# Kernel tuning notes

Measured on AMD Instinct MI355X. Metric: run time of the kernel, lower is better.

The kernel has to match this reference:

```python
import jax, jax.numpy as jnp
import numpy as np


def setup_inputs() -> dict:
    key = jax.random.key(0)
    ks = jax.random.split(key, 7)
    B, T, C, H = 8, 2048, 2048, 128
    x = jax.random.normal(ks[0], (B, T, C), dtype=jnp.float32)
    Wq = jax.random.normal(ks[1], (C, H), dtype=jnp.float32) * (C ** -0.5)
    bq = jax.random.normal(ks[2], (H,), dtype=jnp.float32) * 0.02
    Wk = jax.random.normal(ks[3], (C, H), dtype=jnp.float32) * (C ** -0.5)
    bk = jax.random.normal(ks[4], (H,), dtype=jnp.float32) * 0.02
    Wv = jax.random.normal(ks[5], (C, H), dtype=jnp.float32) * (C ** -0.5)
    bv = jax.random.normal(ks[6], (H,), dtype=jnp.float32) * 0.02
    return {"x": x, "Wq": Wq, "bq": bq, "Wk": Wk, "bk": bk, "Wv": Wv, "bv": bv}


def reference(x, Wq, bq, Wk, bk, Wv, bv):
    # Single-head causal self-attention (dropout in eval mode = identity).
    B, T, C = x.shape
    H = Wq.shape[1]
    Q = jnp.einsum("btc,ch->bth", x, Wq) + bq  # [B,T,H]
    K = jnp.einsum("btc,ch->bth", x, Wk) + bk
    V = jnp.einsum("btc,ch->bth", x, Wv) + bv
    scale = H ** -0.5
    wei = jnp.einsum("bth,bsh->bts", Q, K) * scale  # [B,T,T]
    causal = jnp.tril(jnp.ones((T, T), dtype=bool))
    wei = jnp.where(causal, wei, -jnp.inf)
    wei = jax.nn.softmax(wei, axis=-1)
    out = jnp.einsum("bts,bsh->bth", wei, V)  # [B,T,H]
    return out
```

## Files before the change

kernel.cpp:

```cpp
#include <hip/hip_runtime.h>

typedef float f32x4 __attribute__((ext_vector_type(4)));
typedef short short8 __attribute__((ext_vector_type(8)));
typedef unsigned short ushort8 __attribute__((ext_vector_type(8)));

#define WS_Q  786432
#define WS_K  2883584
#define WS_VT 4980736
#define NITER 64

__device__ __forceinline__ unsigned short f2bf(float x) {
    unsigned u = __float_as_uint(x);
    u += 0x7FFFu + ((u >> 16) & 1u);
    return (unsigned short)(u >> 16);
}

__device__ __forceinline__ int swz128(int row, int cbyte) {
    return row * 128 + (cbyte ^ ((row & 7) << 4));
}

__global__ __launch_bounds__(256) void wt_kernel(const float* __restrict__ Wq,
        const float* __restrict__ Wk, const float* __restrict__ Wv,
        unsigned short* __restrict__ ws) {
    __shared__ __align__(16) unsigned short tile[64][136];
    int mat = blockIdx.x >> 5, ct = blockIdx.x & 31;
    const float* W = (mat == 0) ? Wq : ((mat == 1) ? Wk : Wv);
    int cbase = ct * 64;
    int tid = threadIdx.x;
#pragma unroll
    for (int p = 0; p < 8; p++) {
        int fidx = p * 256 + tid;
        int row = fidx >> 5;
        int c4 = (fidx & 31) << 2;
        float4 v = *(const float4*)&W[(size_t)(cbase + row) * 128 + c4];
        tile[row][c4 + 0] = f2bf(v.x);
        tile[row][c4 + 1] = f2bf(v.y);
        tile[row][c4 + 2] = f2bf(v.z);
        tile[row][c4 + 3] = f2bf(v.w);
    }
    __syncthreads();
    int h = tid >> 1, seg = tid & 1;
    unsigned short* dst = ws + mat * 262144 + (ct * 2 + seg) * 4096 + h * 32;
#pragma unroll
    for (int q4 = 0; q4 < 4; q4++) {
        ushort8 pk;
#pragma unroll
        for (int e = 0; e < 8; e++) pk[e] = tile[seg * 32 + q4 * 8 + e][h];
        *(ushort8*)(dst + q4 * 8) = pk;
    }
}

__global__ __launch_bounds__(256, 3) void qkv_kernel(const float* __restrict__ x,
        const float* __restrict__ bq, const float* __restrict__ bk,
        const float* __restrict__ bv, unsigned short* __restrict__ ws) {
    __shared__ __align__(16) unsigned short lds[4][6144];
    int bid = blockIdx.x;
    int g = bid / 24, j = bid - g * 24;
    int which = j >> 3;
    int mt = g * 8 + (j & 7);
    const unsigned short* WTt = ws + which * 262144;
    const float* x0 = x + (size_t)mt * 64 * 2048;
    int tid = threadIdx.x, lane = tid & 63, wid = tid >> 6;
    int lr = lane & 15, lg = lane >> 4;
    int m0 = (wid >> 1) * 32, n0 = (wid & 1) * 64;

    const float* bias = (which == 0) ? bq : ((which == 1) ? bk : bv);
    float bb[4];
#pragma unroll
    for (int j2 = 0; j2 < 4; j2++) bb[j2] = bias[n0 + j2 * 16 + lr];
    asm volatile("" : "+v"(bb[0]), "+v"(bb[1]), "+v"(bb[2]), "+v"(bb[3]));

    int rowA = tid >> 2, ca = tid & 3;
    const float* aSrc = x0 + (size_t)rowA * 2048 + ca * 8;
    int aDst = rowA * 64 + ((ca ^ ((rowA >> 1) & 3)) << 4);

    int bsrc0, bsrc1, bdst0, bdst1;
    {
        int idx0 = (0 * 4 + wid) * 64 + lane;
        int h0 = idx0 >> 2, c0 = idx0 & 3;
        bsrc0 = h0 * 32 + ((c0 ^ ((h0 >> 1) & 3)) << 3);
        bdst0 = (0 * 4 + wid) * 1024;
        int idx1 = (1 * 4 + wid) * 64 + lane;
        int h1 = idx1 >> 2, c1 = idx1 & 3;
        bsrc1 = h1 * 32 + ((c1 ^ ((h1 >> 1) & 3)) << 3);
        bdst1 = (1 * 4 + wid) * 1024;
    }

    int aOff0, aOff1, bOff0, bOff1, bOff2, bOff3;
    {
        int r0 = m0 + 0 * 16 + lr; aOff0 = r0 * 64 + ((lg ^ ((r0 >> 1) & 3)) << 4);
        int r1 = m0 + 1 * 16 + lr; aOff1 = r1 * 64 + ((lg ^ ((r1 >> 1) & 3)) << 4);
        int s0 = n0 + 0 * 16 + lr; bOff0 = s0 * 64 + ((lg ^ ((s0 >> 1) & 3)) << 4);
        int s1 = n0 + 1 * 16 + lr; bOff1 = s1 * 64 + ((lg ^ ((s1 >> 1) & 3)) << 4);
        int s2 = n0 + 2 * 16 + lr; bOff2 = s2 * 64 + ((lg ^ ((s2 >> 1) & 3)) << 4);
        int s3 = n0 + 3 * 16 + lr; bOff3 = s3 * 64 + ((lg ^ ((s3 >> 1) & 3)) << 4);
    }

    f32x4 acc[2][4];
#pragma unroll
    for (int i = 0; i < 2; i++)
#pragma unroll
        for (int j3 = 0; j3 < 4; j3++) acc[i][j3] = (f32x4){0.f, 0.f, 0.f, 0.f};
    float4 rA[2][2];

#define ISSUE_A(PAR, T) do { \
        const float* ap_ = aSrc + (T) * 32; \
        rA[PAR][0] = *(const float4*)ap_; \
        rA[PAR][1] = *(const float4*)(ap_ + 4); \
    } while (0)
#define ISSUE_B(BUF, T) do { \
        const unsigned short* bs_ = WTt + (size_t)(T) * 4096; \
        char* bd_ = (char*)&lds[BUF][2048]; \
        __builtin_amdgcn_global_load_lds((const __attribute__((address_space(1))) unsigned*)(bs_ + bsrc0), \
            (__attribute__((address_space(3))) unsigned*)(bd_ + bdst0), 16, 0, 0); \
        __builtin_amdgcn_global_load_lds((const __attribute__((address_space(1))) unsigned*)(bs_ + bsrc1), \
            (__attribute__((address_space(3))) unsigned*)(bd_ + bdst1), 16, 0, 0); \
    } while (0)
#define WRITE_A(PAR, BUF) do { \
        const float* f_ = (const float*)&rA[PAR][0]; \
        ushort8 pk_; \
        pk_[0] = f2bf(f_[0]); pk_[1] = f2bf(f_[1]); pk_[2] = f2bf(f_[2]); pk_[3] = f2bf(f_[3]); \
        pk_[4] = f2bf(f_[4]); pk_[5] = f2bf(f_[5]); pk_[6] = f2bf(f_[6]); pk_[7] = f2bf(f_[7]); \
        *(ushort8*)((char*)&lds[BUF][0] + aDst) = pk_; \
    } while (0)

#define QKV_BODY(U, T, STAGE, WRITE, BAR) do { \
        const char* Ab_ = (const char*)&lds[U][0]; \
        const char* Bb_ = (const char*)&lds[U][2048]; \
        short8 av0 = *(const short8*)(Ab_ + aOff0); \
        short8 av1 = *(const short8*)(Ab_ + aOff1); \
        short8 bv0 = *(const short8*)(Bb_ + bOff0); \
        short8 bv1 = *(const short8*)(Bb_ + bOff1); \
        short8 bv2 = *(const short8*)(Bb_ + bOff2); \
        short8 bv3 = *(const short8*)(Bb_ + bOff3); \
        if (STAGE) { ISSUE_A((U) & 1, (T) + 2); ISSUE_B(((U) + 2) & 3, (T) + 2); } \
        acc[0][0] = __builtin_amdgcn_mfma_f32_16x16x32_bf16(av0, bv0, acc[0][0], 0, 0, 0); \
        acc[0][1] = __builtin_amdgcn_mfma_f32_16x16x32_bf16(av0, bv1, acc[0][1], 0, 0, 0); \
        acc[0][2] = __builtin_amdgcn_mfma_f32_16x16x32_bf16(av0, bv2, acc[0][2], 0, 0, 0); \
        acc[0][3] = __builtin_amdgcn_mfma_f32_16x16x32_bf16(av0, bv3, acc[0][3], 0, 0, 0); \
        acc[1][0] = __builtin_amdgcn_mfma_f32_16x16x32_bf16(av1, bv0, acc[1][0], 0, 0, 0); \
        acc[1][1] = __builtin_amdgcn_mfma_f32_16x16x32_bf16(av1, bv1, acc[1][1], 0, 0, 0); \
        acc[1][2] = __builtin_amdgcn_mfma_f32_16x16x32_bf16(av1, bv2, acc[1][2], 0, 0, 0); \
        acc[1][3] = __builtin_amdgcn_mfma_f32_16x16x32_bf16(av1, bv3, acc[1][3], 0, 0, 0); \
        if (STAGE) { asm volatile("s_waitcnt vmcnt(4)" ::: "memory"); } \
        else if (WRITE) { asm volatile("s_waitcnt vmcnt(0)" ::: "memory"); } \
        if (WRITE) { \
            WRITE_A(((U) + 1) & 1, ((U) + 1) & 3); \
            asm volatile("s_waitcnt lgkmcnt(0)" ::: "memory"); \
        } \
        if (BAR) __builtin_amdgcn_s_barrier(); \
    } while (0)

    ISSUE_A(0, 0);
    ISSUE_B(0, 0);
    ISSUE_A(1, 1);
    ISSUE_B(1, 1);
    asm volatile("s_waitcnt vmcnt(4)" ::: "memory");
    WRITE_A(0, 0);
    asm volatile("s_waitcnt lgkmcnt(0)" ::: "memory");
    __builtin_amdgcn_s_barrier();

    for (int to = 0; to < 15; to++) {
        int T0 = to * 4;
        QKV_BODY(0, T0 + 0, true, true, true);
        QKV_BODY(1, T0 + 1, true, true, true);
        QKV_BODY(2, T0 + 2, true, true, true);
        QKV_BODY(3, T0 + 3, true, true, true);
    }
    QKV_BODY(0, 60, true,  true,  true);
    QKV_BODY(1, 61, true,  true,  true);
    QKV_BODY(2, 62, false, true,  true);
    QKV_BODY(3, 63, false, false, false);

    if (which < 2) {
        unsigned short* outp = ws + ((which == 0) ? WS_Q : WS_K);
        float sc = (which == 0) ? 0.08838834764831845f : 1.0f;
#pragma unroll
        for (int i = 0; i < 2; i++)
#pragma unroll
            for (int j3 = 0; j3 < 4; j3++) {
                int h = n0 + j3 * 16 + lr;
#pragma unroll
                for (int r = 0; r < 4; r++) {
                    int t = mt * 64 + m0 + i * 16 + (lg << 2) + r;
                    outp[(size_t)t * 128 + h] = f2bf((acc[i][j3][r] + bb[j3]) * sc);
                }
            }
    } else {
        __syncthreads();
        unsigned short* sm = &lds[0][0];
#pragma unroll
        for (int i = 0; i < 2; i++)
#pragma unroll
            for (int j3 = 0; j3 < 4; j3++) {
                int h = n0 + j3 * 16 + lr;
#pragma unroll
                for (int r = 0; r < 4; r++) {
                    int tl = m0 + i * 16 + (lg << 2) + r;
                    sm[tl * 136 + h] = f2bf(acc[i][j3][r] + bb[j3]);
                }
            }
        __syncthreads();
        int h = tid & 127, seg = tid >> 7;
        int b2 = mt >> 5;
        int tin = (mt & 31) * 64 + seg * 32;
        unsigned short* vt = ws + WS_VT + ((size_t)b2 * 128 + h) * 2048 + tin;
#pragma unroll
        for (int q4 = 0; q4 < 4; q4++) {
            ushort8 pk;
#pragma unroll
            for (int e = 0; e < 8; e++) pk[e] = sm[(seg * 32 + q4 * 8 + e) * 136 + h];
            *(ushort8*)(vt + q4 * 8) = pk;
        }
    }
#undef QKV_BODY
#undef WRITE_A
#undef ISSUE_B
#undef ISSUE_A
}

__global__ __launch_bounds__(256, 2) void attn_kernel(const unsigned short* __restrict__ ws,
        float* __restrict__ out) {
    __shared__ __align__(16) float o_lds[4][32][128];
    __shared__ float ml[4][2][32];
    int b = blockIdx.x;
    int qi = 63 - (int)blockIdx.y;
    int qbase = qi * 32;
    int tid = threadIdx.x, lane = tid & 63, w = tid >> 6;
    int lr = lane & 15, lg = lane >> 4;
    const unsigned short* Qb = ws + WS_Q + (size_t)b * 2048 * 128;
    const unsigned short* Kb = ws + WS_K + (size_t)b * 2048 * 128;
    const unsigned short* Vt = ws + WS_VT + (size_t)b * 128 * 2048;
    char* p_lds = (char*)&o_lds[w][0][0];

    short8 qf[2][4];
#pragma unroll
    for (int i = 0; i < 2; i++)
#pragma unroll
        for (int kf = 0; kf < 4; kf++)
            qf[i][kf] = *(const short8*)&Qb[(size_t)(qbase + i * 16 + lr) * 128 + kf * 32 + lg * 8];

    f32x4 o[2][8];
#pragma unroll
    for (int i = 0; i < 2; i++)
#pragma unroll
        for (int jn = 0; jn < 8; jn++) o[i][jn] = (f32x4){0.f, 0.f, 0.f, 0.f};
    float mrow[2][4], lrow[2][4];
#pragma unroll
    for (int i = 0; i < 2; i++)
#pragma unroll
        for (int r = 0; r < 4; r++) { mrow[i][r] = -__builtin_inff(); lrow[i][r] = 0.f; }

    int ntiles = qi / 2 + 1;
    for (int ti = w; ti < ntiles; ti += 4) {
        int sb = ti * 64;
        f32x4 s[2][4];
#pragma unroll
        for (int i = 0; i < 2; i++)
#pragma unroll
            for (int nf = 0; nf < 4; nf++) s[i][nf] = (f32x4){0.f, 0.f, 0.f, 0.f};
        {
            short8 kb[4][4];
#pragma unroll
            for (int nf = 0; nf < 4; nf++)
#pragma unroll
                for (int kf = 0; kf < 4; kf++)
                    kb[nf][kf] = *(const short8*)&Kb[(size_t)(sb + nf * 16 + lr) * 128 + kf * 32 + lg * 8];
#pragma unroll
            for (int kf = 0; kf < 4; kf++)
#pragma unroll
                for (int i = 0; i < 2; i++)
#pragma unroll
                    for (int nf = 0; nf < 4; nf++)
                        s[i][nf] = __builtin_amdgcn_mfma_f32_16x16x32_bf16(qf[i][kf], kb[nf][kf], s[i][nf], 0, 0, 0);
        }
        if (sb + 63 > qbase) {
#pragma unroll
            for (int i = 0; i < 2; i++)
#pragma unroll
                for (int nf = 0; nf < 4; nf++)
#pragma unroll
                    for (int r = 0; r < 4; r++) {
                        int sg = sb + nf * 16 + lr;
                        int qg = qbase + i * 16 + (lg << 2) + r;
                        if (sg > qg) s[i][nf][r] = -__builtin_inff();
                    }
        }
        float alpha[2][4];
#pragma unroll
        for (int i = 0; i < 2; i++)
#pragma unroll
            for (int r = 0; r < 4; r++) {
                float pm = fmaxf(fmaxf(s[i][0][r], s[i][1][r]), fmaxf(s[i][2][r], s[i][3][r]));
                pm = fmaxf(pm, __shfl_xor(pm, 1));
                pm = fmaxf(pm, __shfl_xor(pm, 2));
                pm = fmaxf(pm, __shfl_xor(pm, 4));
                pm = fmaxf(pm, __shfl_xor(pm, 8));
                float mn = fmaxf(mrow[i][r], pm);
                alpha[i][r] = __expf(mrow[i][r] - mn);
                mrow[i][r] = mn;
            }
#pragma unroll
        for (int i = 0; i < 2; i++)
#pragma unroll
            for (int r = 0; r < 4; r++) {
                float rs = 0.f;
#pragma unroll
                for (int nf = 0; nf < 4; nf++) {
                    float p = __expf(s[i][nf][r] - mrow[i][r]);
                    s[i][nf][r] = p;
                    rs += p;
                }
                rs += __shfl_xor(rs, 1);
                rs += __shfl_xor(rs, 2);
                rs += __shfl_xor(rs, 4);
                rs += __shfl_xor(rs, 8);
                lrow[i][r] = lrow[i][r] * alpha[i][r] + rs;
            }
#pragma unroll
        for (int i = 0; i < 2; i++)
#pragma unroll
            for (int jn = 0; jn < 8; jn++)
#pragma unroll
                for (int r = 0; r < 4; r++) o[i][jn][r] *= alpha[i][r];
#pragma unroll
        for (int i = 0; i < 2; i++)
#pragma unroll
            for (int nf = 0; nf < 4; nf++)
#pragma unroll
                for (int r = 0; r < 4; r++) {
                    int row = i * 16 + (lg << 2) + r;
                    int cb2 = (nf * 16 + lr) * 2;
                    *(unsigned short*)(p_lds + swz128(row, cb2)) = f2bf(s[i][nf][r]);
                }
        asm volatile("s_waitcnt lgkmcnt(0)" ::: "memory");
        short8 pa[2][2];
#pragma unroll
        for (int i = 0; i < 2; i++)
#pragma unroll
            for (int kf = 0; kf < 2; kf++)
                pa[i][kf] = *(const short8*)(p_lds + swz128(i * 16 + lr, kf * 64 + lg * 16));
        short8 vb[8][2];
#pragma unroll
        for (int nf = 0; nf < 8; nf++)
#pragma unroll
            for (int kf = 0; kf < 2; kf++)
                vb[nf][kf] = *(const short8*)&Vt[(size_t)(nf * 16 + lr) * 2048 + sb + kf * 32 + lg * 8];
#pragma unroll
        for (int i = 0; i < 2; i++)
#pragma unroll
            for (int nf = 0; nf < 8; nf++)
#pragma unroll
                for (int kf = 0; kf < 2; kf++)
                    o[i][nf] = __builtin_amdgcn_mfma_f32_16x16x32_bf16(pa[i][kf], vb[nf][kf], o[i][nf], 0, 0, 0);
    }
#pragma unroll
    for (int i = 0; i < 2; i++)
#pragma unroll
        for (int r = 0; r < 4; r++) {
            int q = i * 16 + (lg << 2) + r;
            ml[w][0][q] = mrow[i][r];
            ml[w][1][q] = lrow[i][r];
        }
    asm volatile("s_waitcnt lgkmcnt(0)" ::: "memory");
#pragma unroll
    for (int i = 0; i < 2; i++)
#pragma unroll
        for (int jn = 0; jn < 8; jn++)
#pragma unroll
            for (int r = 0; r < 4; r++)
                o_lds[w][i * 16 + (lg << 2) + r][jn * 16 + lr] = o[i][jn][r];
    __syncthreads();
    int q = tid >> 3, h0 = (tid & 7) << 4;
    float mg = fmaxf(fmaxf(ml[0][0][q], ml[1][0][q]), fmaxf(ml[2][0][q], ml[3][0][q]));
    float scw[4], den = 0.f;
#pragma unroll
    for (int w4 = 0; w4 < 4; w4++) {
        scw[w4] = __expf(ml[w4][0][q] - mg);
        den += scw[w4] * ml[w4][1][q];
    }
    float inv = 1.0f / den;
    float* op = out + ((size_t)b * 2048 + qbase + q) * 128 + h0;
#pragma unroll
    for (int jj = 0; jj < 4; jj++) {
        f32x4 a4 = (f32x4){0.f, 0.f, 0.f, 0.f};
#pragma unroll
        for (int w4 = 0; w4 < 4; w4++) {
            f32x4 v = *(const f32x4*)&o_lds[w4][q][h0 + jj * 4];
            a4 += scw[w4] * v;
        }
        a4 *= inv;
        *(f32x4*)(op + jj * 4) = a4;
    }
}

extern "C" void kernel_launch(void* const* d_in, const int* in_sizes, int n_in,
                              void* d_out, int out_size, void* d_ws, size_t ws_size,
                              hipStream_t stream) {
    (void)in_sizes; (void)n_in; (void)out_size; (void)ws_size;
    const float* x  = (const float*)d_in[0];
    const float* Wq = (const float*)d_in[1];
    const float* bq = (const float*)d_in[2];
    const float* Wk = (const float*)d_in[3];
    const float* bk = (const float*)d_in[4];
    const float* Wv = (const float*)d_in[5];
    const float* bv = (const float*)d_in[6];
    unsigned short* ws = (unsigned short*)d_ws;
    float* out = (float*)d_out;

    wt_kernel<<<96, 256, 0, stream>>>(Wq, Wk, Wv, ws);
    qkv_kernel<<<768, 256, 0, stream>>>(x, bq, bk, bv, ws);
    attn_kernel<<<dim3(8, 64), 256, 0, stream>>>(ws, out);
}
```

Measured before the change: 107.5 us.

## Fuse Q/K/V projections into one block per row tile to reuse x loads

The QKV projection kernel now computes all three outputs (Q, K, V) for a 64-row tile in a single 512-thread block, instead of launching separate blocks per matrix. The goal is to read and convert each x tile from fp32 to bf16 once rather than three times, cutting global traffic on the dominant input. To feed this, the weights are re-laid out interleaved per K-chunk and the LDS pipeline becomes triple-buffered with larger stages. The cost is fewer blocks (256 vs 768), which lowers parallelism and occupancy headroom.

```diff
diff --git a/kernel.cpp b/kernel.cpp
--- a/kernel.cpp
+++ b/kernel.cpp
@@ -3,11 +3,11 @@
 typedef float f32x4 __attribute__((ext_vector_type(4)));
 typedef short short8 __attribute__((ext_vector_type(8)));
 typedef unsigned short ushort8 __attribute__((ext_vector_type(8)));
+typedef unsigned short ushort4v __attribute__((ext_vector_type(4)));
 
 #define WS_Q  786432
 #define WS_K  2883584
 #define WS_VT 4980736
-#define NITER 64
 
 __device__ __forceinline__ unsigned short f2bf(float x) {
     unsigned u = __float_as_uint(x);
@@ -40,7 +40,7 @@
     }
     __syncthreads();
     int h = tid >> 1, seg = tid & 1;
-    unsigned short* dst = ws + mat * 262144 + (ct * 2 + seg) * 4096 + h * 32;
+    unsigned short* dst = ws + (ct * 2 + seg) * 12288 + mat * 4096 + h * 32;
 #pragma unroll
     for (int q4 = 0; q4 < 4; q4++) {
         ushort8 pk;
@@ -50,169 +50,147 @@
     }
 }
 
-__global__ __launch_bounds__(256, 3) void qkv_kernel(const float* __restrict__ x,
+__global__ __launch_bounds__(512, 2) void qkv_kernel(const float* __restrict__ x,
         const float* __restrict__ bq, const float* __restrict__ bk,
         const float* __restrict__ bv, unsigned short* __restrict__ ws) {
-    __shared__ __align__(16) unsigned short lds[4][6144];
-    int bid = blockIdx.x;
-    int g = bid / 24, j = bid - g * 24;
-    int which = j >> 3;
-    int mt = g * 8 + (j & 7);
-    const unsigned short* WTt = ws + which * 262144;
+    __shared__ __align__(16) char lds_raw[3 * 28672];
+    int mt = blockIdx.x;
+    const unsigned short* WTt = ws;
     const float* x0 = x + (size_t)mt * 64 * 2048;
-    int tid = threadIdx.x, lane = tid & 63, wid = tid >> 6;
+    int tid = threadIdx.x, lane = tid & 63, w = tid >> 6;
     int lr = lane & 15, lg = lane >> 4;
-    int m0 = (wid >> 1) * 32, n0 = (wid & 1) * 64;
-
-    const float* bias = (which == 0) ? bq : ((which == 1) ? bk : bv);
-    float bb[4];
-#pragma unroll
-    for (int j2 = 0; j2 < 4; j2++) bb[j2] = bias[n0 + j2 * 16 + lr];
-    asm volatile("" : "+v"(bb[0]), "+v"(bb[1]), "+v"(bb[2]), "+v"(bb[3]));
-
-    int rowA = tid >> 2, ca = tid & 3;
-    const float* aSrc = x0 + (size_t)rowA * 2048 + ca * 8;
-    int aDst = rowA * 64 + ((ca ^ ((rowA >> 1) & 3)) << 4);
-
-    int bsrc0, bsrc1, bdst0, bdst1;
-    {
-        int idx0 = (0 * 4 + wid) * 64 + lane;
-        int h0 = idx0 >> 2, c0 = idx0 & 3;
-        bsrc0 = h0 * 32 + ((c0 ^ ((h0 >> 1) & 3)) << 3);
-        bdst0 = (0 * 4 + wid) * 1024;
-        int idx1 = (1 * 4 + wid) * 64 + lane;
-        int h1 = idx1 >> 2, c1 = idx1 & 3;
-        bsrc1 = h1 * 32 + ((c1 ^ ((h1 >> 1) & 3)) << 3);
-        bdst1 = (1 * 4 + wid) * 1024;
-    }
-
-    int aOff0, aOff1, bOff0, bOff1, bOff2, bOff3;
-    {
-        int r0 = m0 + 0 * 16 + lr; aOff0 = r0 * 64 + ((lg ^ ((r0 >> 1) & 3)) << 4);
-        int r1 = m0 + 1 * 16 + lr; aOff1 = r1 * 64 + ((lg ^ ((r1 >> 1) & 3)) << 4);
-        int s0 = n0 + 0 * 16 + lr; bOff0 = s0 * 64 + ((lg ^ ((s0 >> 1) & 3)) << 4);
-        int s1 = n0 + 1 * 16 + lr; bOff1 = s1 * 64 + ((lg ^ ((s1 >> 1) & 3)) << 4);
-        int s2 = n0 + 2 * 16 + lr; bOff2 = s2 * 64 + ((lg ^ ((s2 >> 1) & 3)) << 4);
-        int s3 = n0 + 3 * 16 + lr; bOff3 = s3 * 64 + ((lg ^ ((s3 >> 1) & 3)) << 4);
-    }
-
-    f32x4 acc[2][4];
-#pragma unroll
-    for (int i = 0; i < 2; i++)
-#pragma unroll
-        for (int j3 = 0; j3 < 4; j3++) acc[i][j3] = (f32x4){0.f, 0.f, 0.f, 0.f};
-    float4 rA[2][2];
-
-#define ISSUE_A(PAR, T) do { \
-        const float* ap_ = aSrc + (T) * 32; \
-        rA[PAR][0] = *(const float4*)ap_; \
-        rA[PAR][1] = *(const float4*)(ap_ + 4); \
+
+    int hme = w * 16 + lr;
+    float bb0 = bq[hme], bb1 = bk[hme], bb2 = bv[hme];
+    asm volatile("" : "+v"(bb0), "+v"(bb1), "+v"(bb2));
+    asm volatile("s_waitcnt vmcnt(0)" ::: "memory");
+
+    int rowA = tid >> 3, kk = tid & 7;
+    const float* aSrc = x0 + (size_t)rowA * 2048 + kk * 4;
+    int aDst = rowA * 64 + (((kk >> 1) ^ (rowA & 3)) << 4) + ((kk & 1) << 3);
+
+    int bOffG[3], bDstC[3];
+#pragma unroll
+    for (int j = 0; j < 3; j++) {
+        int c = j * 8 + w;
+        int r = c * 16 + (lane >> 2);
+        int s = (lane & 3) ^ (r & 3);
+        bOffG[j] = r * 32 + s * 8;
+        bDstC[j] = c * 1024;
+    }
+
+    int xorT = (lg ^ (lr & 3)) << 4;
+    int aOff[4], bOff[3];
+#pragma unroll
+    for (int i = 0; i < 4; i++) aOff[i] = (i * 16 + lr) * 64 + xorT;
+#pragma unroll
+    for (int j = 0; j < 3; j++) bOff[j] = ((j * 8 + w) * 16 + lr) * 64 + xorT;
+
+    f32x4 acc[4][3];
+#pragma unroll
+    for (int i = 0; i < 4; i++)
+#pragma unroll
+        for (int j = 0; j < 3; j++) acc[i][j] = (f32x4){0.f, 0.f, 0.f, 0.f};
+    float4 rA[2];
+
+#define ISSUE_A(T) do { rA[(T) & 1] = *(const float4*)(aSrc + (size_t)(T) * 32); } while (0)
+#define ISSUE_B(BUF, T) do { \
+        const unsigned short* bs_ = WTt + (size_t)(T) * 12288; \
+        char* bd_ = lds_raw + (BUF) * 28672 + 4096; \
+        __builtin_amdgcn_global_load_lds((const __attribute__((address_space(1))) unsigned*)(bs_ + bOffG[0]), \
+            (__attribute__((address_space(3))) unsigned*)(bd_ + bDstC[0]), 16, 0, 0); \
+        __builtin_amdgcn_global_load_lds((const __attribute__((address_space(1))) unsigned*)(bs_ + bOffG[1]), \
+            (__attribute__((address_space(3))) unsigned*)(bd_ + bDstC[1]), 16, 0, 0); \
+        __builtin_amdgcn_global_load_lds((const __attribute__((address_space(1))) unsigned*)(bs_ + bOffG[2]), \
+            (__attribute__((address_space(3))) unsigned*)(bd_ + bDstC[2]), 16, 0, 0); \
     } while (0)
-#define ISSUE_B(BUF, T) do { \
-        const unsigned short* bs_ = WTt + (size_t)(T) * 4096; \
-        char* bd_ = (char*)&lds[BUF][2048]; \
-        __builtin_amdgcn_global_load_lds((const __attribute__((address_space(1))) unsigned*)(bs_ + bsrc0), \
-            (__attribute__((address_space(3))) unsigned*)(bd_ + bdst0), 16, 0, 0); \
-        __builtin_amdgcn_global_load_lds((const __attribute__((address_space(1))) unsigned*)(bs_ + bsrc1), \
-            (__attribute__((address_space(3))) unsigned*)(bd_ + bdst1), 16, 0, 0); \
+#define WRITE_A(T, BUF) do { \
+        const float* f_ = (const float*)&rA[(T) & 1]; \
+        ushort4v pk_; \
+        pk_[0] = f2bf(f_[0]); pk_[1] = f2bf(f_[1]); pk_[2] = f2bf(f_[2]); pk_[3] = f2bf(f_[3]); \
+        *(ushort4v*)(lds_raw + (BUF) * 28672 + aDst) = pk_; \
     } while (0)
-#define WRITE_A(PAR, BUF) do { \
-        const float* f_ = (const float*)&rA[PAR][0]; \
-        ushort8 pk_; \
-        pk_[0] = f2bf(f_[0]); pk_[1] = f2bf(f_[1]); pk_[2] = f2bf(f_[2]); pk_[3] = f2bf(f_[3]); \
-        pk_[4] = f2bf(f_[4]); pk_[5] = f2bf(f_[5]); pk_[6] = f2bf(f_[6]); pk_[7] = f2bf(f_[7]); \
-        *(ushort8*)((char*)&lds[BUF][0] + aDst) = pk_; \
-    } while (0)
 
 #define QKV_BODY(U, T, STAGE, WRITE, BAR) do { \
-        const char* Ab_ = (const char*)&lds[U][0]; \
-        const char* Bb_ = (const char*)&lds[U][2048]; \
-        short8 av0 = *(const short8*)(Ab_ + aOff0); \
-        short8 av1 = *(const short8*)(Ab_ + aOff1); \
-        short8 bv0 = *(const short8*)(Bb_ + bOff0); \
-        short8 bv1 = *(const short8*)(Bb_ + bOff1); \
-        short8 bv2 = *(const short8*)(Bb_ + bOff2); \
-        short8 bv3 = *(const short8*)(Bb_ + bOff3); \
-        if (STAGE) { ISSUE_A((U) & 1, (T) + 2); ISSUE_B(((U) + 2) & 3, (T) + 2); } \
+        const char* Ab_ = lds_raw + (U) * 28672; \
+        const char* Bb_ = Ab_ + 4096; \
+        short8 av0 = *(const short8*)(Ab_ + aOff[0]); \
+        short8 av1 = *(const short8*)(Ab_ + aOff[1]); \
+        short8 av2 = *(const short8*)(Ab_ + aOff[2]); \
+        short8 av3 = *(const short8*)(Ab_ + aOff[3]); \
+        short8 bv0 = *(const short8*)(Bb_ + bOff[0]); \
+        short8 bv1 = *(const short8*)(Bb_ + bOff[1]); \
+        short8 bv2 = *(const short8*)(Bb_ + bOff[2]); \
+        if (STAGE) { ISSUE_A((T) + 2); ISSUE_B(((U) + 2) % 3, (T) + 2); } \
         acc[0][0] = __builtin_amdgcn_mfma_f32_16x16x32_bf16(av0, bv0, acc[0][0], 0, 0, 0); \
+        acc[1][0] = __builtin_amdgcn_mfma_f32_16x16x32_bf16(av1, bv0, acc[1][0], 0, 0, 0); \
+        acc[2][0] = __builtin_amdgcn_mfma_f32_16x16x32_bf16(av2, bv0, acc[2][0], 0, 0, 0); \
+        acc[3][0] = __builtin_amdgcn_mfma_f32_16x16x32_bf16(av3, bv0, acc[3][0], 0, 0, 0); \
         acc[0][1] = __builtin_amdgcn_mfma_f32_16x16x32_bf16(av0, bv1, acc[0][1], 0, 0, 0); \
+        acc[1][1] = __builtin_amdgcn_mfma_f32_16x16x32_bf16(av1, bv1, acc[1][1], 0, 0, 0); \
+        acc[2][1] = __builtin_amdgcn_mfma_f32_16x16x32_bf16(av2, bv1, acc[2][1], 0, 0, 0); \
+        acc[3][1] = __builtin_amdgcn_mfma_f32_16x16x32_bf16(av3, bv1, acc[3][1], 0, 0, 0); \
         acc[0][2] = __builtin_amdgcn_mfma_f32_16x16x32_bf16(av0, bv2, acc[0][2], 0, 0, 0); \
-        acc[0][3] = __builtin_amdgcn_mfma_f32_16x16x32_bf16(av0, bv3, acc[0][3], 0, 0, 0); \
-        acc[1][0] = __builtin_amdgcn_mfma_f32_16x16x32_bf16(av1, bv0, acc[1][0], 0, 0, 0); \
-        acc[1][1] = __builtin_amdgcn_mfma_f32_16x16x32_bf16(av1, bv1, acc[1][1], 0, 0, 0); \
         acc[1][2] = __builtin_amdgcn_mfma_f32_16x16x32_bf16(av1, bv2, acc[1][2], 0, 0, 0); \
-        acc[1][3] = __builtin_amdgcn_mfma_f32_16x16x32_bf16(av1, bv3, acc[1][3], 0, 0, 0); \
+        acc[2][2] = __builtin_amdgcn_mfma_f32_16x16x32_bf16(av2, bv2, acc[2][2], 0, 0, 0); \
+        acc[3][2] = __builtin_amdgcn_mfma_f32_16x16x32_bf16(av3, bv2, acc[3][2], 0, 0, 0); \
         if (STAGE) { asm volatile("s_waitcnt vmcnt(4)" ::: "memory"); } \
         else if (WRITE) { asm volatile("s_waitcnt vmcnt(0)" ::: "memory"); } \
         if (WRITE) { \
-            WRITE_A(((U) + 1) & 1, ((U) + 1) & 3); \
+            WRITE_A((T) + 1, ((U) + 1) % 3); \
             asm volatile("s_waitcnt lgkmcnt(0)" ::: "memory"); \
         } \
         if (BAR) __builtin_amdgcn_s_barrier(); \
     } while (0)
 
-    ISSUE_A(0, 0);
-    ISSUE_B(0, 0);
-    ISSUE_A(1, 1);
-    ISSUE_B(1, 1);
+    ISSUE_A(0); ISSUE_B(0, 0);
+    ISSUE_A(1); ISSUE_B(1, 1);
     asm volatile("s_waitcnt vmcnt(4)" ::: "memory");
     WRITE_A(0, 0);
     asm volatile("s_waitcnt lgkmcnt(0)" ::: "memory");
     __builtin_amdgcn_s_barrier();
 
-    for (int to = 0; to < 15; to++) {
-        int T0 = to * 4;
+    for (int t3 = 0; t3 < 20; t3++) {
+        int T0 = t3 * 3;
         QKV_BODY(0, T0 + 0, true, true, true);
         QKV_BODY(1, T0 + 1, true, true, true);
         QKV_BODY(2, T0 + 2, true, true, true);
-        QKV_BODY(3, T0 + 3, true, true, true);
     }
     QKV_BODY(0, 60, true,  true,  true);
     QKV_BODY(1, 61, true,  true,  true);
     QKV_BODY(2, 62, false, true,  true);
-    QKV_BODY(3, 63, false, false, false);
-
-    if (which < 2) {
-        unsigned short* outp = ws + ((which == 0) ? WS_Q : WS_K);
-        float sc = (which == 0) ? 0.08838834764831845f : 1.0f;
-#pragma unroll
-        for (int i = 0; i < 2; i++)
-#pragma unroll
-            for (int j3 = 0; j3 < 4; j3++) {
-                int h = n0 + j3 * 16 + lr;
-#pragma unroll
-                for (int r = 0; r < 4; r++) {
-                    int t = mt * 64 + m0 + i * 16 + (lg << 2) + r;
-                    outp[(size_t)t * 128 + h] = f2bf((acc[i][j3][r] + bb[j3]) * sc);
-                }
-            }
-    } else {
-        __syncthreads();
-        unsigned short* sm = &lds[0][0];
-#pragma unroll
-        for (int i = 0; i < 2; i++)
-#pragma unroll
-            for (int j3 = 0; j3 < 4; j3++) {
-                int h = n0 + j3 * 16 + lr;
-#pragma unroll
-                for (int r = 0; r < 4; r++) {
-                    int tl = m0 + i * 16 + (lg << 2) + r;
-                    sm[tl * 136 + h] = f2bf(acc[i][j3][r] + bb[j3]);
-                }
-            }
-        __syncthreads();
-        int h = tid & 127, seg = tid >> 7;
-        int b2 = mt >> 5;
-        int tin = (mt & 31) * 64 + seg * 32;
-        unsigned short* vt = ws + WS_VT + ((size_t)b2 * 128 + h) * 2048 + tin;
-#pragma unroll
-        for (int q4 = 0; q4 < 4; q4++) {
-            ushort8 pk;
-#pragma unroll
-            for (int e = 0; e < 8; e++) pk[e] = sm[(seg * 32 + q4 * 8 + e) * 136 + h];
-            *(ushort8*)(vt + q4 * 8) = pk;
-        }
-    }
+    QKV_BODY(0, 63, false, false, false);
+
+    __syncthreads();
+    unsigned short* qout = ws + WS_Q;
+    unsigned short* kout = ws + WS_K;
+    const float sc = 0.08838834764831845f;
+#pragma unroll
+    for (int i = 0; i < 4; i++)
+#pragma unroll
+        for (int r = 0; r < 4; r++) {
+            size_t t = (size_t)mt * 64 + i * 16 + (lg << 2) + r;
+            qout[t * 128 + hme] = f2bf((acc[i][0][r] + bb0) * sc);
+            kout[t * 128 + hme] = f2bf(acc[i][1][r] + bb1);
+        }
+    unsigned short* vt_sm = (unsigned short*)lds_raw;
+#pragma unroll
+    for (int i = 0; i < 4; i++)
+#pragma unroll
+        for (int r = 0; r < 4; r++)
+            vt_sm[(i * 16 + (lg << 2) + r) * 136 + hme] = f2bf(acc[i][2][r] + bb2);
+    __syncthreads();
+    int h2 = tid >> 2, q4 = tid & 3;
+    unsigned short* vdst = ws + WS_VT + ((size_t)(mt >> 5) * 128 + h2) * 2048
+                           + (mt & 31) * 64 + q4 * 16;
+    ushort8 pk0, pk1;
+#pragma unroll
+    for (int e = 0; e < 8; e++) {
+        pk0[e] = vt_sm[(q4 * 16 + e) * 136 + h2];
+        pk1[e] = vt_sm[(q4 * 16 + 8 + e) * 136 + h2];
+    }
+    *(ushort8*)vdst = pk0;
+    *(ushort8*)(vdst + 8) = pk1;
 #undef QKV_BODY
 #undef WRITE_A
 #undef ISSUE_B
@@ -409,6 +387,6 @@
     float* out = (float*)d_out;
 
     wt_kernel<<<96, 256, 0, stream>>>(Wq, Wk, Wv, ws);
-    qkv_kernel<<<768, 256, 0, stream>>>(x, bq, bk, bv, ws);
+    qkv_kernel<<<256, 512, 0, stream>>>(x, bq, bk, bv, ws);
     attn_kernel<<<dim3(8, 64), 256, 0, stream>>>(ws, out);
 }
```

After: 131.7 us. 22.5% more time.
